# Kernel tuning notes

Measured on AMD Instinct MI355X. Metric: run time of the kernel, lower is better.

The kernel has to match this reference:

```python
import jax, jax.numpy as jnp
import numpy as np

B, DK, N, DV = 16, 64, 8192, 64


def setup_inputs() -> dict:
    key = jax.random.key(0)
    kq, kk, kv = jax.random.split(key, 3)
    q = jax.random.normal(kq, (B, DK, N), dtype=jnp.float32)   # channel-first q
    k = jax.random.normal(kk, (B, N, DK), dtype=jnp.float32)
    v = jax.random.normal(kv, (B, N, DV), dtype=jnp.float32)
    return {"q": q, "k": k, "v": v}


def reference(q, k, v):
    # torch: bmm(q.permute(0,2,1), bmm(k.permute(0,2,1), v))
    # k^T v: [B, DK, DV] -- small on-chip-able intermediate
    ktv = jnp.einsum('bnk,bnv->bkv', k, v)
    # q^T (k^T v): [B, N, DV]
    out = jnp.einsum('bkn,bkv->bnv', q, ktv)
    return out
```

## Files before the change

kernel.cpp:

```cpp
#include <hip/hip_runtime.h>


#define B_   16
#define N_   8192
#define DK_  64
#define DV_  64
#define CH_  64

__global__ __launch_bounds__(256) void p1_partial(
    const float* __restrict__ K, const float* __restrict__ V,
    float* __restrict__ part)
{
    __shared__ float sm[4][2048];

    const int c = blockIdx.x, b = blockIdx.y, t = threadIdx.x;
    const int w = t >> 6, lane = t & 63;
    const int kk = (lane >> 3) * 8;
    const int vv = (lane & 7) * 8;
    float* Ksw = &sm[w][0];
    float* Vsw = &sm[w][1024];

    const size_t row0 = (size_t)b * N_ + (size_t)c * 128 + (size_t)w * 32;
    const float4* K4 = (const float4*)(K + row0 * DK_);
    const float4* V4 = (const float4*)(V + row0 * DV_);

    float acc[8][8] = {};

    #pragma unroll
    for (int r = 0; r < 2; ++r) {
        float4 kb_[4], vb_[4];
        #pragma unroll
        for (int j = 0; j < 4; ++j) kb_[j] = K4[r * 256 + j * 64 + lane];
        #pragma unroll
        for (int j = 0; j < 4; ++j) vb_[j] = V4[r * 256 + j * 64 + lane];
        #pragma unroll
        for (int j = 0; j < 4; ++j) {
            ((float4*)Ksw)[j * 64 + lane] = kb_[j];
            ((float4*)Vsw)[j * 64 + lane] = vb_[j];
        }
        #pragma unroll 4
        for (int n = 0; n < 16; ++n) {
            alignas(16) float fk[8], fv[8];
            *(float4*)&fk[0] = *(const float4*)&Ksw[n * 64 + kk];
            *(float4*)&fk[4] = *(const float4*)&Ksw[n * 64 + kk + 4];
            *(float4*)&fv[0] = *(const float4*)&Vsw[n * 64 + vv];
            *(float4*)&fv[4] = *(const float4*)&Vsw[n * 64 + vv + 4];
            #pragma unroll
            for (int i = 0; i < 8; ++i)
                #pragma unroll
                for (int j = 0; j < 8; ++j)
                    acc[i][j] += fk[i] * fv[j];
        }
    }

    __syncthreads();
    float* red = &sm[0][0];
    if (w == 0) {
        #pragma unroll
        for (int i = 0; i < 8; ++i) {
            *(float4*)&red[(kk + i) * 64 + vv]     = make_float4(acc[i][0], acc[i][1], acc[i][2], acc[i][3]);
            *(float4*)&red[(kk + i) * 64 + vv + 4] = make_float4(acc[i][4], acc[i][5], acc[i][6], acc[i][7]);
        }
    }
    __syncthreads();
    #pragma unroll
    for (int ww = 1; ww < 4; ++ww) {
        if (w == ww) {
            #pragma unroll
            for (int i = 0; i < 8; ++i) {
                float4 r0 = *(float4*)&red[(kk + i) * 64 + vv];
                float4 r1 = *(float4*)&red[(kk + i) * 64 + vv + 4];
                r0.x += acc[i][0]; r0.y += acc[i][1]; r0.z += acc[i][2]; r0.w += acc[i][3];
                r1.x += acc[i][4]; r1.y += acc[i][5]; r1.z += acc[i][6]; r1.w += acc[i][7];
                *(float4*)&red[(kk + i) * 64 + vv]     = r0;
                *(float4*)&red[(kk + i) * 64 + vv + 4] = r1;
            }
        }
        __syncthreads();
    }

    float4* P = (float4*)(part + ((size_t)c * B_ + b) * 4096);
    #pragma unroll
    for (int j = 0; j < 4; ++j)
        P[t + 256 * j] = ((const float4*)red)[t + 256 * j];
}

__global__ __launch_bounds__(256) void p1_reduce(
    const float* __restrict__ part, float* __restrict__ ktv)
{
    const int idx = blockIdx.x * 256 + threadIdx.x;
    float s = 0.f;
    #pragma unroll 16
    for (int c = 0; c < CH_; ++c)
        s += part[(size_t)c * 65536 + idx];
    ktv[idx] = s;
}

__global__ __launch_bounds__(256) void p2(
    const float* __restrict__ q, const float* __restrict__ ktv,
    float* __restrict__ out)
{
    __shared__ float ks[4096];

    const int nb = blockIdx.x, b = blockIdx.y, t = threadIdx.x;
    const int w = t >> 6, lane = t & 63;
    const int nl = (lane >> 3) * 4;
    const int vl = (lane & 7) * 8;
    const int n0 = nb * 128 + w * 32;

    const float4* kt4 = (const float4*)(ktv + (size_t)b * 4096);
    #pragma unroll
    for (int j = 0; j < 4; ++j)
        ((float4*)ks)[t + 256 * j] = kt4[t + 256 * j];
    __syncthreads();

    const float* ql = q + (size_t)b * DK_ * N_ + n0 + nl;

    float acc[4][8] = {};
    #pragma unroll
    for (int kb = 0; kb < 4; ++kb) {
        alignas(16) float fq[16][4];
        #pragma unroll
        for (int u = 0; u < 16; ++u)
            *(float4*)&fq[u][0] = *(const float4*)(ql + (size_t)(kb * 16 + u) * N_);
        #pragma unroll
        for (int u = 0; u < 16; ++u) {
            const int k = kb * 16 + u;
            alignas(16) float fv[8];
            *(float4*)&fv[0] = *(const float4*)&ks[k * 64 + vl];
            *(float4*)&fv[4] = *(const float4*)&ks[k * 64 + vl + 4];
            #pragma unroll
            for (int i = 0; i < 4; ++i)
                #pragma unroll
                for (int j = 0; j < 8; ++j)
                    acc[i][j] += fq[u][i] * fv[j];
        }
    }

    float* ob = out + ((size_t)b * N_ + n0 + nl) * DV_ + vl;
    #pragma unroll
    for (int i = 0; i < 4; ++i) {
        *(float4*)&ob[(size_t)i * DV_]     = make_float4(acc[i][0], acc[i][1], acc[i][2], acc[i][3]);
        *(float4*)&ob[(size_t)i * DV_ + 4] = make_float4(acc[i][4], acc[i][5], acc[i][6], acc[i][7]);
    }
}

extern "C" void kernel_launch(void* const* d_in, const int* in_sizes, int n_in,
                              void* d_out, int out_size, void* d_ws, size_t ws_size,
                              hipStream_t stream)
{
    (void)in_sizes; (void)n_in; (void)out_size; (void)ws_size;
    const float* q = (const float*)d_in[0];
    const float* k = (const float*)d_in[1];
    const float* v = (const float*)d_in[2];
    float* out = (float*)d_out;

    float* part = (float*)d_ws;
    float* ktv  = part + (size_t)CH_ * B_ * 4096;

    p1_partial<<<dim3(CH_, B_), 256, 0, stream>>>(k, v, part);
    p1_reduce<<<dim3(256), 256, 0, stream>>>(part, ktv);
    p2<<<dim3(64, B_), 256, 0, stream>>>(q, ktv, out);
}
```

Measured before the change: 150.0 us.

## Fuse partial reduction into p1 via last-block atomic counter; hoist q loads in p2

Removes the separate p1_reduce kernel. Each p1_partial block bumps a per-batch atomic counter, and the last block to finish sums the 64 partials for that batch into ktv. A hipMemsetAsync clears the counters on every launch. In p2, the first q tile is loaded before the shared-memory barrier, which overlaps the global q reads with the ktv staging. The fusion saves a kernel launch, but the final reduction now runs serially in one block per batch, and a memset is added to each call.

```diff
diff --git a/kernel.cpp b/kernel.cpp
--- a/kernel.cpp
+++ b/kernel.cpp
@@ -9,9 +9,10 @@
 
 __global__ __launch_bounds__(256) void p1_partial(
     const float* __restrict__ K, const float* __restrict__ V,
-    float* __restrict__ part)
+    float* __restrict__ part, float* __restrict__ ktv, int* __restrict__ cnt)
 {
     __shared__ float sm[4][2048];
+    __shared__ int last;
 
     const int c = blockIdx.x, b = blockIdx.y, t = threadIdx.x;
     const int w = t >> 6, lane = t & 63;
@@ -83,17 +84,28 @@
     #pragma unroll
     for (int j = 0; j < 4; ++j)
         P[t + 256 * j] = ((const float4*)red)[t + 256 * j];
-}
 
-__global__ __launch_bounds__(256) void p1_reduce(
-    const float* __restrict__ part, float* __restrict__ ktv)
-{
-    const int idx = blockIdx.x * 256 + threadIdx.x;
-    float s = 0.f;
-    #pragma unroll 16
-    for (int c = 0; c < CH_; ++c)
-        s += part[(size_t)c * 65536 + idx];
-    ktv[idx] = s;
+    __syncthreads();
+    if (t == 0) {
+        __threadfence();
+        last = (atomicAdd(&cnt[b], 1) == CH_ - 1);
+    }
+    __syncthreads();
+    if (last) {
+        const float4* Pa = (const float4*)part;
+        float4* Kt = (float4*)(ktv + (size_t)b * 4096);
+        float4 s0 = {0,0,0,0}, s1 = {0,0,0,0}, s2 = {0,0,0,0}, s3 = {0,0,0,0};
+        #pragma unroll 8
+        for (int cc = 0; cc < CH_; ++cc) {
+            const float4* Pc = Pa + ((size_t)cc * B_ + b) * 1024;
+            const float4 a0 = Pc[t], a1 = Pc[t + 256], a2 = Pc[t + 512], a3 = Pc[t + 768];
+            s0.x += a0.x; s0.y += a0.y; s0.z += a0.z; s0.w += a0.w;
+            s1.x += a1.x; s1.y += a1.y; s1.z += a1.z; s1.w += a1.w;
+            s2.x += a2.x; s2.y += a2.y; s2.z += a2.z; s2.w += a2.w;
+            s3.x += a3.x; s3.y += a3.y; s3.z += a3.z; s3.w += a3.w;
+        }
+        Kt[t] = s0; Kt[t + 256] = s1; Kt[t + 512] = s2; Kt[t + 768] = s3;
+    }
 }
 
 __global__ __launch_bounds__(256) void p2(
@@ -112,17 +124,19 @@
     #pragma unroll
     for (int j = 0; j < 4; ++j)
         ((float4*)ks)[t + 256 * j] = kt4[t + 256 * j];
-    __syncthreads();
 
     const float* ql = q + (size_t)b * DK_ * N_ + n0 + nl;
+
+    alignas(16) float fq[16][4];
+    #pragma unroll
+    for (int u = 0; u < 16; ++u)
+        *(float4*)&fq[u][0] = *(const float4*)(ql + (size_t)u * N_);
+
+    __syncthreads();
 
     float acc[4][8] = {};
     #pragma unroll
     for (int kb = 0; kb < 4; ++kb) {
-        alignas(16) float fq[16][4];
-        #pragma unroll
-        for (int u = 0; u < 16; ++u)
-            *(float4*)&fq[u][0] = *(const float4*)(ql + (size_t)(kb * 16 + u) * N_);
         #pragma unroll
         for (int u = 0; u < 16; ++u) {
             const int k = kb * 16 + u;
@@ -134,6 +148,12 @@
                 #pragma unroll
                 for (int j = 0; j < 8; ++j)
                     acc[i][j] += fq[u][i] * fv[j];
+        }
+        if (kb + 1 < 4) {
+            #pragma unroll
+            for (int u = 0; u < 16; ++u)
+                *(float4*)&fq[u][0] =
+                    *(const float4*)(ql + (size_t)((kb + 1) * 16 + u) * N_);
         }
     }
 
@@ -157,8 +177,9 @@
 
     float* part = (float*)d_ws;
     float* ktv  = part + (size_t)CH_ * B_ * 4096;
+    int*   cnt  = (int*)(ktv + (size_t)B_ * 4096);
 
-    p1_partial<<<dim3(CH_, B_), 256, 0, stream>>>(k, v, part);
-    p1_reduce<<<dim3(256), 256, 0, stream>>>(part, ktv);
+    hipMemsetAsync(cnt, 0, B_ * sizeof(int), stream);
+    p1_partial<<<dim3(CH_, B_), 256, 0, stream>>>(k, v, part, ktv, cnt);
     p2<<<dim3(64, B_), 256, 0, stream>>>(q, ktv, out);
 }
```

New measurement: 218.4 us. 45.6% more time.
